# Performance work log

Measured on AMD Instinct MI355X. Metric: run time of the kernel, lower is better.

The kernel has to match this reference:

```python
import jax, jax.numpy as jnp
import numpy as np

B, N = 128, 1024


def setup_inputs() -> dict:
    key = jax.random.key(0)
    k1, k2 = jax.random.split(key)
    vector = jax.random.uniform(k1, (B, N), dtype=jnp.float32)
    interactions = jax.random.normal(k2, (N, N), dtype=jnp.float32)
    return {"vector": vector, "interactions": interactions}


def reference(vector, interactions):
    # x: [B,1,N], y: [B,N,1] -> broadcast dirac delta [B,N,N]
    x = vector[:, None, :]
    y = vector[:, :, None]
    dd = (1.0 - x) * (1.0 - y) + x * y  # [B,N,N]
    dd = jnp.triu(dd)                   # keep upper triangle incl. diagonal
    energy = dd * interactions          # [B,N,N] * [N,N] broadcast
    return energy.reshape(vector.shape[0], -1).sum(axis=1)  # [B]
```

## Files before the change

### kernel.cpp

```cpp
#include <hip/hip_runtime.h>

#define NDIM 1024
#define BDIM 128
#define TS 32
#define NT (NDIM / TS)
#define NTILES (NT * (NT + 1) / 2)

__global__ __launch_bounds__(256) void potts_main(
    const float* __restrict__ V,
    const float* __restrict__ W,
    float* __restrict__ partial)
{
    const int t = blockIdx.x;
    int ti = 0, rem = t;
    while (rem >= NT - ti) { rem -= NT - ti; ++ti; }
    const int tj = ti + rem;
    const int I0 = ti * TS, J0 = tj * TS;
    const bool diag = (ti == tj);

    __shared__ float wt[TS][36];
    __shared__ float rs[TS];
    __shared__ float vjt[TS][130];
    __shared__ float vit[TS][130];
    __shared__ float red[4][BDIM];

    const int tid = threadIdx.x;
    const int w = tid >> 6;
    const int l = tid & 63;

    {
        const int r = tid >> 3, c4 = (tid & 7) * 4;
        float4 w4 = *(const float4*)(W + (size_t)(I0 + r) * NDIM + (J0 + c4));
        if (diag) {
            if (c4 + 0 < r) w4.x = 0.0f;
            if (c4 + 1 < r) w4.y = 0.0f;
            if (c4 + 2 < r) w4.z = 0.0f;
            if (c4 + 3 < r) w4.w = 0.0f;
        }
        *(float4*)(&wt[r][c4]) = w4;
        float rsum = (w4.x + w4.y) + (w4.z + w4.w);
        rsum += __shfl_xor(rsum, 1);
        rsum += __shfl_xor(rsum, 2);
        rsum += __shfl_xor(rsum, 4);
        if ((tid & 7) == 0) rs[r] = rsum;
    }

    for (int it = 0; it < 2; ++it) {
        const int task = tid + 256 * it;
        const int p = task >> 3, g = task & 7;
        {
            const float4 a = *(const float4*)(V + (size_t)(2 * p) * NDIM + J0 + 4 * g);
            const float4 c = *(const float4*)(V + (size_t)(2 * p + 1) * NDIM + J0 + 4 * g);
            *(float2*)(&vjt[4 * g + 0][2 * p]) = make_float2(a.x, c.x);
            *(float2*)(&vjt[4 * g + 1][2 * p]) = make_float2(a.y, c.y);
            *(float2*)(&vjt[4 * g + 2][2 * p]) = make_float2(a.z, c.z);
            *(float2*)(&vjt[4 * g + 3][2 * p]) = make_float2(a.w, c.w);
        }
        {
            const float4 a = *(const float4*)(V + (size_t)(2 * p) * NDIM + I0 + 4 * g);
            const float4 c = *(const float4*)(V + (size_t)(2 * p + 1) * NDIM + I0 + 4 * g);
            *(float2*)(&vit[4 * g + 0][2 * p]) = make_float2(a.x, c.x);
            *(float2*)(&vit[4 * g + 1][2 * p]) = make_float2(a.y, c.y);
            *(float2*)(&vit[4 * g + 2][2 * p]) = make_float2(a.z, c.z);
            *(float2*)(&vit[4 * g + 3][2 * p]) = make_float2(a.w, c.w);
        }
    }
    __syncthreads();

    float vj0[TS], vj1[TS];
#pragma unroll
    for (int j = 0; j < TS; ++j) {
        const float2 p2 = *(const float2*)(&vjt[j][2 * l]);
        vj0[j] = p2.x;
        vj1[j] = p2.y;
    }

    float acc0 = 0.0f, acc1 = 0.0f;
#pragma unroll
    for (int k = 0; k < 8; ++k) {
        const int i = 8 * w + k;
        const float2 vi2 = *(const float2*)(&vit[i][2 * l]);
        const float q0 = 1.0f - vi2.x, r0 = 2.0f * vi2.x - 1.0f;
        const float q1 = 1.0f - vi2.y, r1 = 2.0f * vi2.y - 1.0f;
        const float* wrow = &wt[i][0];
        float za0 = 0.f, zb0 = 0.f, za1 = 0.f, zb1 = 0.f;
#pragma unroll
        for (int j4 = 0; j4 < 8; j4 += 2) {
            const float4 wa = *(const float4*)(wrow + 4 * j4);
            const float4 wb = *(const float4*)(wrow + 4 * j4 + 4);
            za0 = fmaf(wa.x, vj0[4 * j4 + 0], za0);
            za0 = fmaf(wa.y, vj0[4 * j4 + 1], za0);
            za0 = fmaf(wa.z, vj0[4 * j4 + 2], za0);
            za0 = fmaf(wa.w, vj0[4 * j4 + 3], za0);
            za1 = fmaf(wa.x, vj1[4 * j4 + 0], za1);
            za1 = fmaf(wa.y, vj1[4 * j4 + 1], za1);
            za1 = fmaf(wa.z, vj1[4 * j4 + 2], za1);
            za1 = fmaf(wa.w, vj1[4 * j4 + 3], za1);
            zb0 = fmaf(wb.x, vj0[4 * j4 + 4], zb0);
            zb0 = fmaf(wb.y, vj0[4 * j4 + 5], zb0);
            zb0 = fmaf(wb.z, vj0[4 * j4 + 6], zb0);
            zb0 = fmaf(wb.w, vj0[4 * j4 + 7], zb0);
            zb1 = fmaf(wb.x, vj1[4 * j4 + 4], zb1);
            zb1 = fmaf(wb.y, vj1[4 * j4 + 5], zb1);
            zb1 = fmaf(wb.z, vj1[4 * j4 + 6], zb1);
            zb1 = fmaf(wb.w, vj1[4 * j4 + 7], zb1);
        }
        const float rsk = rs[i];
        acc0 = fmaf(q0, rsk, acc0);
        acc0 = fmaf(r0, za0 + zb0, acc0);
        acc1 = fmaf(q1, rsk, acc1);
        acc1 = fmaf(r1, za1 + zb1, acc1);
    }

    *(float2*)(&red[w][2 * l]) = make_float2(acc0, acc1);
    __syncthreads();
    if (tid < BDIM) {
        partial[t * BDIM + tid] =
            (red[0][tid] + red[1][tid]) + (red[2][tid] + red[3][tid]);
    }
}

__global__ __launch_bounds__(64) void potts_red(
    const float* __restrict__ partial, float* __restrict__ out)
{
    const int b = blockIdx.x;
    const int lane = threadIdx.x;
    float a0 = 0.f, a1 = 0.f;
    int t = lane;
#pragma unroll 4
    for (; t + 64 < NTILES; t += 128) {
        a0 += partial[t * BDIM + b];
        a1 += partial[(t + 64) * BDIM + b];
    }
    if (t < NTILES) a0 += partial[t * BDIM + b];
    float a = a0 + a1;
#pragma unroll
    for (int off = 32; off > 0; off >>= 1)
        a += __shfl_down(a, off);
    if (lane == 0) out[b] = a;
}

extern "C" void kernel_launch(void* const* d_in, const int* in_sizes, int n_in,
                              void* d_out, int out_size, void* d_ws, size_t ws_size,
                              hipStream_t stream) {
    const float* V = (const float*)d_in[0];
    const float* W = (const float*)d_in[1];
    float* out = (float*)d_out;
    float* partial = (float*)d_ws;

    potts_main<<<dim3(NTILES), dim3(256), 0, stream>>>(V, W, partial);
    potts_red<<<dim3(BDIM), dim3(64), 0, stream>>>(partial, out);
}
```

Measured before the change: 64.20 us.

## Fuse partial reduction into main kernel via atomic last-block counter

Drops the second reduction kernel. Each tile block writes per-wave partials in a batch-major layout and bumps a global atomic counter. The last 128 blocks to arrive spin until all tiles finish, then each sums one batch row. This removes a kernel launch and makes the final reads contiguous. In exchange it adds a memset, a busy-wait that assumes forward progress of the other blocks, and four times more partial data in the workspace.

```diff
diff --git a/kernel.cpp b/kernel.cpp
--- a/kernel.cpp
+++ b/kernel.cpp
@@ -5,11 +5,16 @@
 #define TS 32
 #define NT (NDIM / TS)
 #define NTILES (NT * (NT + 1) / 2)
+#define PSTRIDE (NTILES * 4)
+#define NRED 128
+#define RED_BASE (NTILES - NRED)
 
-__global__ __launch_bounds__(256) void potts_main(
+__global__ __launch_bounds__(256) void potts_fused(
     const float* __restrict__ V,
     const float* __restrict__ W,
-    float* __restrict__ partial)
+    float* __restrict__ partial,
+    unsigned* __restrict__ cnt,
+    float* __restrict__ out)
 {
     const int t = blockIdx.x;
     int ti = 0, rem = t;
@@ -22,7 +27,7 @@
     __shared__ float rs[TS];
     __shared__ float vjt[TS][130];
     __shared__ float vit[TS][130];
-    __shared__ float red[4][BDIM];
+    __shared__ unsigned sOld;
 
     const int tid = threadIdx.x;
     const int w = tid >> 6;
@@ -112,32 +117,42 @@
         acc1 = fmaf(r1, za1 + zb1, acc1);
     }
 
-    *(float2*)(&red[w][2 * l]) = make_float2(acc0, acc1);
+    const int col = 4 * t + w;
+    partial[(size_t)(2 * l) * PSTRIDE + col] = acc0;
+    partial[(size_t)(2 * l + 1) * PSTRIDE + col] = acc1;
+
     __syncthreads();
-    if (tid < BDIM) {
-        partial[t * BDIM + tid] =
-            (red[0][tid] + red[1][tid]) + (red[2][tid] + red[3][tid]);
+    if (tid == 0) {
+        __threadfence();
+        sOld = __hip_atomic_fetch_add(cnt, 1u, __ATOMIC_ACQ_REL,
+                                      __HIP_MEMORY_SCOPE_AGENT);
     }
-}
+    __syncthreads();
 
-__global__ __launch_bounds__(64) void potts_red(
-    const float* __restrict__ partial, float* __restrict__ out)
-{
-    const int b = blockIdx.x;
-    const int lane = threadIdx.x;
-    float a0 = 0.f, a1 = 0.f;
-    int t = lane;
-#pragma unroll 4
-    for (; t + 64 < NTILES; t += 128) {
-        a0 += partial[t * BDIM + b];
-        a1 += partial[(t + 64) * BDIM + b];
+    if (sOld >= RED_BASE) {
+        const int slot = (int)(sOld - RED_BASE);
+        if (tid == 0) {
+            while (__hip_atomic_load(cnt, __ATOMIC_ACQUIRE,
+                                     __HIP_MEMORY_SCOPE_AGENT) < NTILES)
+                __builtin_amdgcn_s_sleep(2);
+            __threadfence();
+        }
+        __syncthreads();
+
+        const float* row = partial + (size_t)slot * PSTRIDE;
+        float s = 0.0f;
+        for (int k4 = tid; k4 < PSTRIDE / 4; k4 += 256) {
+            const float4 p = *(const float4*)(row + 4 * k4);
+            s += (p.x + p.y) + (p.z + p.w);
+        }
+#pragma unroll
+        for (int off = 32; off > 0; off >>= 1)
+            s += __shfl_down(s, off);
+        if (l == 0) rs[w] = s;
+        __syncthreads();
+        if (tid == 0)
+            out[slot] = (rs[0] + rs[1]) + (rs[2] + rs[3]);
     }
-    if (t < NTILES) a0 += partial[t * BDIM + b];
-    float a = a0 + a1;
-#pragma unroll
-    for (int off = 32; off > 0; off >>= 1)
-        a += __shfl_down(a, off);
-    if (lane == 0) out[b] = a;
 }
 
 extern "C" void kernel_launch(void* const* d_in, const int* in_sizes, int n_in,
@@ -147,7 +162,8 @@
     const float* W = (const float*)d_in[1];
     float* out = (float*)d_out;
     float* partial = (float*)d_ws;
+    unsigned* cnt = (unsigned*)(partial + (size_t)BDIM * PSTRIDE);
 
-    potts_main<<<dim3(NTILES), dim3(256), 0, stream>>>(V, W, partial);
-    potts_red<<<dim3(BDIM), dim3(64), 0, stream>>>(partial, out);
+    hipMemsetAsync((void*)cnt, 0, sizeof(unsigned), stream);
+    potts_fused<<<dim3(NTILES), dim3(256), 0, stream>>>(V, W, partial, cnt, out);
 }
```

Measured after the change: 107.6 us. 1.68x slower.
